# Kernel tuning notes

Measured on AMD Instinct MI355X. Metric: run time of the kernel, lower is better.

Reference implementation:

```python
import jax, jax.numpy as jnp
import numpy as np

B, T, D, C = 8, 4096, 768, 2048

def setup_inputs() -> dict:
    key = jax.random.key(0)
    k1, k2 = jax.random.split(key)
    embed = jax.random.normal(k1, (B, T, D), dtype=jnp.float32)
    cluster_centers = jax.random.normal(k2, (C, D), dtype=jnp.float32)
    return {"embed": embed, "cluster_centers": cluster_centers}

def reference(embed, cluster_centers):
    x_sq = jnp.sum(embed * embed, axis=-1, keepdims=True)          # (b, t, 1)
    c_sq = jnp.sum(cluster_centers * cluster_centers, axis=-1)     # (c,)
    cross = jnp.einsum('btd,cd->btc', embed, cluster_centers)      # (b, t, c)
    sq_dists = x_sq + c_sq[None, None, :] - 2.0 * cross
    dists = jnp.sqrt(jnp.maximum(sq_dists, 0.0))
    # dists argmax of -cdist == argmin of cdist
    clusters = jnp.argmin(dists, axis=-1)                          # (b, t) int
    return clusters
```

## Files before the change

kernel.cpp:

```cpp
#include <hip/hip_runtime.h>

typedef __fp16 f16x2 __attribute__((ext_vector_type(2)));
typedef __fp16 f16x8 __attribute__((ext_vector_type(8)));
typedef float f32x4 __attribute__((ext_vector_type(4)));

constexpr int MM = 32768;
constexpr int NN = 2048;
constexpr int KK = 768;
constexpr int BM = 128;
constexpr int BN = 128;
constexpr int NKT = KK / 32;
constexpr int NA_UNITS = (MM / 16) * NKT;
constexpr int NB_UNITS = (NN / 16) * NKT;

constexpr size_t WS_APACK = 0;
constexpr size_t WS_BPACK = WS_APACK + (size_t)MM * KK * 4;
constexpr size_t WS_CSQ   = WS_BPACK + (size_t)NN * KK * 4;
constexpr size_t WS_SLOT  = WS_CSQ + (size_t)NN * 4;
constexpr size_t WS_NEED  = WS_SLOT + (size_t)MM * 16 * 8;

__device__ __forceinline__ unsigned bc(f16x2 h) {
    return __builtin_bit_cast(unsigned, h);
}


__global__ __launch_bounds__(256)
void fragpack_kernel(const float* __restrict__ A, const float* __restrict__ Bc,
                     uint4* __restrict__ Ap, uint4* __restrict__ Bp,
                     float* __restrict__ csq) {
    const int task = blockIdx.x * 4 + (threadIdx.x >> 6);
    const int lane = threadIdx.x & 63;

    if (task >= NA_UNITS + NB_UNITS) {
        const int cl = task - (NA_UNITS + NB_UNITS);
        const float4* row = reinterpret_cast<const float4*>(Bc + (size_t)cl * KK);
        float s = 0.f;
#pragma unroll
        for (int w = 0; w < KK / (4 * 64); ++w) {
            float4 v = row[w * 64 + lane];
            s = fmaf(v.x, v.x, s); s = fmaf(v.y, v.y, s);
            s = fmaf(v.z, v.z, s); s = fmaf(v.w, v.w, s);
        }
#pragma unroll
        for (int off = 32; off > 0; off >>= 1) s += __shfl_xor(s, off, 64);
        if (lane == 0) csq[cl] = s;
        return;
    }

    const int ln15 = lane & 15;
    const int quad = lane >> 4;

    const bool isB = task >= NA_UNITS;
    const int t = isB ? task - NA_UNITS : task;
    const int tile = t / NKT, kt = t % NKT;
    const float* src = (isB ? Bc : A) + (size_t)(tile * 16 + ln15) * KK + kt * 32 + quad * 8;
    uint4* dst = (isB ? Bp : Ap) + (size_t)t * 128 + lane;

    const float4 v0 = *(const float4*)(src);
    const float4 v1 = *(const float4*)(src + 4);
    f16x2 h0 = __builtin_amdgcn_cvt_pkrtz(v0.x, v0.y);
    f16x2 h1 = __builtin_amdgcn_cvt_pkrtz(v0.z, v0.w);
    f16x2 h2 = __builtin_amdgcn_cvt_pkrtz(v1.x, v1.y);
    f16x2 h3 = __builtin_amdgcn_cvt_pkrtz(v1.z, v1.w);
    f16x2 l0 = __builtin_amdgcn_cvt_pkrtz(v0.x-(float)h0[0], v0.y-(float)h0[1]);
    f16x2 l1 = __builtin_amdgcn_cvt_pkrtz(v0.z-(float)h1[0], v0.w-(float)h1[1]);
    f16x2 l2 = __builtin_amdgcn_cvt_pkrtz(v1.x-(float)h2[0], v1.y-(float)h2[1]);
    f16x2 l3 = __builtin_amdgcn_cvt_pkrtz(v1.z-(float)h3[0], v1.w-(float)h3[1]);
    uint4 hv = {bc(h0), bc(h1), bc(h2), bc(h3)};
    uint4 lv = {bc(l0), bc(l1), bc(l2), bc(l3)};
    dst[0]  = hv;
    dst[64] = lv;
}

__global__ __launch_bounds__(64)
void csq_kernel(const float* __restrict__ cc, float* __restrict__ csq) {
    const int cl = blockIdx.x;
    const int lane = threadIdx.x;
    const float4* row = reinterpret_cast<const float4*>(cc + (size_t)cl * KK);
    float s = 0.f;
#pragma unroll
    for (int w = 0; w < KK / (4 * 64); ++w) {
        float4 v = row[w * 64 + lane];
        s = fmaf(v.x, v.x, s); s = fmaf(v.y, v.y, s);
        s = fmaf(v.z, v.z, s); s = fmaf(v.w, v.w, s);
    }
#pragma unroll
    for (int off = 32; off > 0; off >>= 1) s += __shfl_xor(s, off, 64);
    if (lane == 0) csq[cl] = s;
}

#define MF(a, b, c) __builtin_amdgcn_mfma_f32_16x16x32_f16( \
    __builtin_bit_cast(f16x8, a), __builtin_bit_cast(f16x8, b), c, 0, 0, 0)

#define COMP_J(Ah_, Al_, Bh_, Bl_, j) \
    _Pragma("unroll") \
    for (int i = 0; i < 4; ++i) { \
        acc[i][j] = MF(Ah_[i], Bh_[j], acc[i][j]); \
        acc[i][j] = MF(Ah_[i], Bl_[j], acc[i][j]); \
        acc[i][j] = MF(Al_[i], Bh_[j], acc[i][j]); \
    }

#define LOAD_B(Bh_, Bl_, kt_) { const int o_ = (kt_) * 128; \
    _Pragma("unroll") \
    for (int j = 0; j < 4; ++j) { Bh_[j] = b_ptr[j][o_]; Bl_[j] = b_ptr[j][o_ + 64]; } }

#define LOAD_A(Ah_, Al_, kt_) { const int o_ = (kt_) * 128; \
    _Pragma("unroll") \
    for (int i = 0; i < 4; ++i) { Ah_[i] = a_ptr[i][o_]; Al_[i] = a_ptr[i][o_ + 64]; } }

__global__ __launch_bounds__(256, 2)
void gemm_pack_kernel(const uint4* __restrict__ Ap, const uint4* __restrict__ Bp,
                      const float* __restrict__ csq, uint2* __restrict__ slots) {
    const int b   = blockIdx.x;
    const int xcd = b & 7;
    const int s   = b >> 3;
    const int gx  = s & 15;
    const int gy  = xcd + ((s >> 4) << 3);

    const int tid  = threadIdx.x;
    const int lane = tid & 63;
    const int ln15 = lane & 15;
    const int quad = lane >> 4;
    const int wave = tid >> 6;
    const int wm = wave >> 1, wn = wave & 1;
    const int tbase = gy * BM;
    const int cb    = gx * BN;

    const uint4* a_ptr[4];
    const uint4* b_ptr[4];
#pragma unroll
    for (int i = 0; i < 4; ++i) {
        a_ptr[i] = Ap + (size_t)(gy * 8 + wm * 4 + i) * NKT * 128 + lane;
        b_ptr[i] = Bp + (size_t)(gx * 8 + wn * 4 + i) * NKT * 128 + lane;
    }

    f32x4 acc[4][4];
#pragma unroll
    for (int i = 0; i < 4; ++i)
#pragma unroll
        for (int j = 0; j < 4; ++j) { f32x4 z = {0.f,0.f,0.f,0.f}; acc[i][j] = z; }

    uint4 Ah0[4], Al0[4], Bh0[4], Bl0[4];
    uint4 Ah1[4], Al1[4], Bh1[4], Bl1[4];

    LOAD_B(Bh0, Bl0, 0)
    LOAD_A(Ah0, Al0, 0)
#pragma unroll 1
    for (int kt = 0; kt < NKT; kt += 2) {
        LOAD_B(Bh1, Bl1, kt + 1)
        COMP_J(Ah0, Al0, Bh0, Bl0, 0)
        COMP_J(Ah0, Al0, Bh0, Bl0, 1)
        LOAD_A(Ah1, Al1, kt + 1)
        COMP_J(Ah0, Al0, Bh0, Bl0, 2)
        COMP_J(Ah0, Al0, Bh0, Bl0, 3)
        if (kt + 2 < NKT) LOAD_B(Bh0, Bl0, kt + 2)
        COMP_J(Ah1, Al1, Bh1, Bl1, 0)
        COMP_J(Ah1, Al1, Bh1, Bl1, 1)
        if (kt + 2 < NKT) LOAD_A(Ah0, Al0, kt + 2)
        COMP_J(Ah1, Al1, Bh1, Bl1, 2)
        COMP_J(Ah1, Al1, Bh1, Bl1, 3)
    }

    float csq4[4];
#pragma unroll
    for (int j = 0; j < 4; ++j) csq4[j] = csq[cb + wn * 64 + j * 16 + ln15];

    float bval[16]; int bidx[16];
#pragma unroll
    for (int i = 0; i < 4; ++i)
#pragma unroll
        for (int r = 0; r < 4; ++r) {
            const int rid = i * 4 + r;
            float bv_ = csq4[0] - 2.0f * acc[i][0][r];
            int   bi_ = cb + wn * 64 + ln15;
#pragma unroll
            for (int j = 1; j < 4; ++j) {
                const float s2 = csq4[j] - 2.0f * acc[i][j][r];
                const int   c = cb + wn * 64 + j * 16 + ln15;
                if (s2 < bv_) { bv_ = s2; bi_ = c; }
            }
            bval[rid] = bv_; bidx[rid] = bi_;
        }
#pragma unroll
    for (int off = 1; off < 16; off <<= 1) {
#pragma unroll
        for (int rid = 0; rid < 16; ++rid) {
            const float ov = __shfl_xor(bval[rid], off, 64);
            const int   oi = __shfl_xor(bidx[rid], off, 64);
            if (ov < bval[rid] || (ov == bval[rid] && oi < bidx[rid])) {
                bval[rid] = ov; bidx[rid] = oi;
            }
        }
    }

    __shared__ float vtab[256];
    __shared__ int   itab[256];
    if (ln15 == 0) {
#pragma unroll
        for (int i = 0; i < 4; ++i)
#pragma unroll
            for (int r = 0; r < 4; ++r) {
                const int row = wm * 64 + i * 16 + quad * 4 + r;
                vtab[row * 2 + wn] = bval[i * 4 + r];
                itab[row * 2 + wn] = bidx[i * 4 + r];
            }
    }
    __syncthreads();
    if (tid < 128) {
        float v0 = vtab[tid * 2]; int i0 = itab[tid * 2];
        const float v1 = vtab[tid * 2 + 1]; const int i1 = itab[tid * 2 + 1];
        if (v1 < v0 || (v1 == v0 && i1 < i0)) { v0 = v1; i0 = i1; }
        uint2 e; e.x = __float_as_uint(v0); e.y = (unsigned)i0;
        slots[(size_t)(tbase + tid) * 16 + gx] = e;
    }
}

__global__ __launch_bounds__(256)
void slot_reduce_kernel(const uint2* __restrict__ slots, int* __restrict__ out) {
    const int t = blockIdx.x * 256 + threadIdx.x;
    const uint2* s = slots + (size_t)t * 16;
    float bv = __uint_as_float(s[0].x); int bi = (int)s[0].y;
#pragma unroll
    for (int j = 1; j < 16; ++j) {
        const uint2 e = s[j];
        const float v = __uint_as_float(e.x);
        if (v < bv || (v == bv && (int)e.y < bi)) { bv = v; bi = (int)e.y; }
    }
    out[t] = bi;
}


__global__ __launch_bounds__(256)
void init_ws_kernel(unsigned long long* __restrict__ w) {
    w[blockIdx.x * 256 + threadIdx.x] = 0xFFFFFFFFFFFFFFFFull;
}

__global__ __launch_bounds__(256, 2)
void argmin_mfma_kernel(const float* __restrict__ A, const float* __restrict__ Bc,
                        const float* __restrict__ csq,
                        unsigned long long* __restrict__ ws64) {
    __shared__ unsigned lds[4 * 128 * 20];
    constexpr int AH = 0, AL = 2560, BH = 5120;

    const int tid  = threadIdx.x;
    const int lane = tid & 63;
    const int ln15 = lane & 15;
    const int quad = lane >> 4;
    const int wave = tid >> 6;
    const int wm = wave >> 1, wn = wave & 1;
    const int tbase = blockIdx.x * BM;
    const int cb    = blockIdx.y * BN;

    const int sr  = tid >> 1;
    const int skh = tid & 1;
    const float* gA = A  + (size_t)(tbase + sr) * KK + skh * 16;
    const float* gB = Bc + (size_t)(cb   + sr) * KK + skh * 16;
    const int wword = sr * 20 + skh * 8;

    f32x4 acc[4][4];
#pragma unroll
    for (int i = 0; i < 4; ++i)
#pragma unroll
        for (int j = 0; j < 4; ++j) { f32x4 z = {0.f,0.f,0.f,0.f}; acc[i][j] = z; }

    float4 av[4], bv[4];
#pragma unroll
    for (int p = 0; p < 4; ++p) {
        av[p] = *(const float4*)(gA + p * 4);
        bv[p] = *(const float4*)(gB + p * 4);
    }

    int aw[4], bw[4];
#pragma unroll
    for (int i = 0; i < 4; ++i) {
        aw[i] = AH + (wm * 64 + i * 16 + ln15) * 20 + quad * 4;
        bw[i] = BH + (wn * 64 + i * 16 + ln15) * 20 + quad * 4;
    }

    for (int k0 = 0; k0 < KK; k0 += 32) {
        __syncthreads();
#pragma unroll
        for (int h = 0; h < 2; ++h) {
            float4 v0 = av[2*h], v1 = av[2*h+1];
            f16x2 h00 = __builtin_amdgcn_cvt_pkrtz(v0.x, v0.y);
            f16x2 h01 = __builtin_amdgcn_cvt_pkrtz(v0.z, v0.w);
            f16x2 h10 = __builtin_amdgcn_cvt_pkrtz(v1.x, v1.y);
            f16x2 h11 = __builtin_amdgcn_cvt_pkrtz(v1.z, v1.w);
            f16x2 l00 = __builtin_amdgcn_cvt_pkrtz(v0.x-(float)h00[0], v0.y-(float)h00[1]);
            f16x2 l01 = __builtin_amdgcn_cvt_pkrtz(v0.z-(float)h01[0], v0.w-(float)h01[1]);
            f16x2 l10 = __builtin_amdgcn_cvt_pkrtz(v1.x-(float)h10[0], v1.y-(float)h10[1]);
            f16x2 l11 = __builtin_amdgcn_cvt_pkrtz(v1.z-(float)h11[0], v1.w-(float)h11[1]);
            uint4 hv = {bc(h00), bc(h01), bc(h10), bc(h11)};
            uint4 lv = {bc(l00), bc(l01), bc(l10), bc(l11)};
            *(uint4*)&lds[AH + wword + 4*h] = hv;
            *(uint4*)&lds[AL + wword + 4*h] = lv;

            float4 w0 = bv[2*h], w1 = bv[2*h+1];
            f16x2 g00 = __builtin_amdgcn_cvt_pkrtz(w0.x, w0.y);
            f16x2 g01 = __builtin_amdgcn_cvt_pkrtz(w0.z, w0.w);
            f16x2 g10 = __builtin_amdgcn_cvt_pkrtz(w1.x, w1.y);
            f16x2 g11 = __builtin_amdgcn_cvt_pkrtz(w1.z, w1.w);
            f16x2 m00 = __builtin_amdgcn_cvt_pkrtz(w0.x-(float)g00[0], w0.y-(float)g00[1]);
            f16x2 m01 = __builtin_amdgcn_cvt_pkrtz(w0.z-(float)g01[0], w0.w-(float)g01[1]);
            f16x2 m10 = __builtin_amdgcn_cvt_pkrtz(w1.x-(float)g10[0], w1.y-(float)g10[1]);
            f16x2 m11 = __builtin_amdgcn_cvt_pkrtz(w1.z-(float)g11[0], w1.w-(float)g11[1]);
            uint4 gv = {bc(g00), bc(g01), bc(g10), bc(g11)};
            uint4 mv = {bc(m00), bc(m01), bc(m10), bc(m11)};
            *(uint4*)&lds[BH + wword + 4*h]        = gv;
            *(uint4*)&lds[BH + 2560 + wword + 4*h] = mv;
        }
        __syncthreads();

        const int kn = k0 + 32;
        if (kn < KK) {
#pragma unroll
            for (int p = 0; p < 4; ++p) {
                av[p] = *(const float4*)(gA + kn + p * 4);
                bv[p] = *(const float4*)(gB + kn + p * 4);
            }
        }

        f16x8 a_h[4], a_l[4], b_h[4], b_l[4];
#pragma unroll
        for (int i = 0; i < 4; ++i) {
            a_h[i] = *(const f16x8*)&lds[aw[i]];
            a_l[i] = *(const f16x8*)&lds[aw[i] + 2560];
            b_h[i] = *(const f16x8*)&lds[bw[i]];
            b_l[i] = *(const f16x8*)&lds[bw[i] + 2560];
        }
#pragma unroll
        for (int i = 0; i < 4; ++i)
#pragma unroll
            for (int j = 0; j < 4; ++j) {
                acc[i][j] = __builtin_amdgcn_mfma_f32_16x16x32_f16(a_h[i], b_h[j], acc[i][j], 0, 0, 0);
                acc[i][j] = __builtin_amdgcn_mfma_f32_16x16x32_f16(a_h[i], b_l[j], acc[i][j], 0, 0, 0);
                acc[i][j] = __builtin_amdgcn_mfma_f32_16x16x32_f16(a_l[i], b_h[j], acc[i][j], 0, 0, 0);
            }
    }

    float csq4[4];
#pragma unroll
    for (int j = 0; j < 4; ++j) csq4[j] = csq[cb + wn * 64 + j * 16 + ln15];

    float bval[16]; int bidx[16];
#pragma unroll
    for (int i = 0; i < 4; ++i)
#pragma unroll
        for (int r = 0; r < 4; ++r) {
            const int rid = i * 4 + r;
            float bv_ = csq4[0] - 2.0f * acc[i][0][r];
            int   bi_ = cb + wn * 64 + ln15;
#pragma unroll
            for (int j = 1; j < 4; ++j) {
                const float s = csq4[j] - 2.0f * acc[i][j][r];
                const int   c = cb + wn * 64 + j * 16 + ln15;
                if (s < bv_) { bv_ = s; bi_ = c; }
            }
            bval[rid] = bv_; bidx[rid] = bi_;
        }
#pragma unroll
    for (int off = 1; off < 16; off <<= 1) {
#pragma unroll
        for (int rid = 0; rid < 16; ++rid) {
            const float ov = __shfl_xor(bval[rid], off, 64);
            const int   oi = __shfl_xor(bidx[rid], off, 64);
            if (ov < bval[rid] || (ov == bval[rid] && oi < bidx[rid])) {
                bval[rid] = ov; bidx[rid] = oi;
            }
        }
    }

    __syncthreads();
    float* vtab = (float*)&lds[0];
    int*   itab = (int*)&lds[256];
    if (ln15 == 0) {
#pragma unroll
        for (int i = 0; i < 4; ++i)
#pragma unroll
            for (int r = 0; r < 4; ++r) {
                const int row = wm * 64 + i * 16 + quad * 4 + r;
                vtab[row * 2 + wn] = bval[i * 4 + r];
                itab[row * 2 + wn] = bidx[i * 4 + r];
            }
    }
    __syncthreads();
    if (tid < 128) {
        float v0 = vtab[tid * 2]; int i0 = itab[tid * 2];
        const float v1 = vtab[tid * 2 + 1]; const int i1 = itab[tid * 2 + 1];
        if (v1 < v0 || (v1 == v0 && i1 < i0)) { v0 = v1; i0 = i1; }
        const unsigned b   = __float_as_uint(v0);
        const unsigned key = (b & 0x80000000u) ? ~b : (b | 0x80000000u);
        const unsigned long long pk =
            ((unsigned long long)key << 32) | (unsigned long long)(unsigned)i0;
        atomicMin(&ws64[tbase + tid], pk);
    }
}

__global__ __launch_bounds__(256)
void unpack_kernel(const unsigned long long* __restrict__ w, int* __restrict__ out) {
    const int i = blockIdx.x * 256 + threadIdx.x;
    out[i] = (int)(unsigned)(w[i] & 0xFFFFFFFFull);
}

extern "C" void kernel_launch(void* const* d_in, const int* in_sizes, int n_in,
                              void* d_out, int out_size, void* d_ws, size_t ws_size,
                              hipStream_t stream) {
    const float* embed   = (const float*)d_in[0];
    const float* centers = (const float*)d_in[1];
    int* out = (int*)d_out;

    if (ws_size >= WS_NEED) {
        uint4* Ap = (uint4*)((char*)d_ws + WS_APACK);
        uint4* Bp = (uint4*)((char*)d_ws + WS_BPACK);
        float* csq   = (float*)((char*)d_ws + WS_CSQ);
        uint2* slots = (uint2*)((char*)d_ws + WS_SLOT);
        fragpack_kernel<<<(NA_UNITS + NB_UNITS + NN) / 4, 256, 0, stream>>>(
            embed, centers, Ap, Bp, csq);
        gemm_pack_kernel<<<(MM / BM) * (NN / BN), 256, 0, stream>>>(
            Ap, Bp, csq, slots);
        slot_reduce_kernel<<<MM / 256, 256, 0, stream>>>(slots, out);
    } else {
        unsigned long long* ws64 = (unsigned long long*)d_ws;
        float* csq = (float*)((char*)d_ws + (size_t)MM * 8);
        init_ws_kernel<<<MM / 256, 256, 0, stream>>>(ws64);
        csq_kernel<<<NN, 64, 0, stream>>>(centers, csq);
        argmin_mfma_kernel<<<dim3(MM / BM, NN / BN), 256, 0, stream>>>(
            embed, centers, csq, ws64);
        unpack_kernel<<<MM / 256, 256, 0, stream>>>(ws64, out);
    }
}
```

Before: 441.2 us.

## Use 256x256 LDS-staged tiles with async global-to-LDS double buffering in GEMM

The packed-fragment GEMM moves from 128x128 tiles, where each wave loads its fragments directly from global memory, to 256x256 tiles with 512 threads. Fragments are staged cooperatively into double-buffered LDS via global_load_lds, and each wave then reads them from LDS to feed the MFMAs. The goal is to cut global/L2 traffic through more reuse per tile and to overlap the next k-tile load with compute, with s_setprio to favour the MFMA issue. The cost is two barriers per k-step, higher register pressure from 8x4 accumulators, and fewer blocks, which may hurt occupancy and load balance. Column slots per row drop from 16 to 8, so the reduce kernel is adjusted to match.

Measured after the change: 429.0 us. 2.8% less time.

```diff
diff --git a/kernel.cpp b/kernel.cpp
--- a/kernel.cpp
+++ b/kernel.cpp
@@ -7,8 +7,6 @@
 constexpr int MM = 32768;
 constexpr int NN = 2048;
 constexpr int KK = 768;
-constexpr int BM = 128;
-constexpr int BN = 128;
 constexpr int NKT = KK / 32;
 constexpr int NA_UNITS = (MM / 16) * NKT;
 constexpr int NB_UNITS = (NN / 16) * NKT;
@@ -17,7 +15,7 @@
 constexpr size_t WS_BPACK = WS_APACK + (size_t)MM * KK * 4;
 constexpr size_t WS_CSQ   = WS_BPACK + (size_t)NN * KK * 4;
 constexpr size_t WS_SLOT  = WS_CSQ + (size_t)NN * 4;
-constexpr size_t WS_NEED  = WS_SLOT + (size_t)MM * 16 * 8;
+constexpr size_t WS_NEED  = WS_SLOT + (size_t)MM * 8 * 8;
 
 __device__ __forceinline__ unsigned bc(f16x2 h) {
     return __builtin_bit_cast(unsigned, h);
@@ -89,33 +87,196 @@
     if (lane == 0) csq[cl] = s;
 }
 
-#define MF(a, b, c) __builtin_amdgcn_mfma_f32_16x16x32_f16( \
-    __builtin_bit_cast(f16x8, a), __builtin_bit_cast(f16x8, b), c, 0, 0, 0)
-
-#define COMP_J(Ah_, Al_, Bh_, Bl_, j) \
-    _Pragma("unroll") \
-    for (int i = 0; i < 4; ++i) { \
-        acc[i][j] = MF(Ah_[i], Bh_[j], acc[i][j]); \
-        acc[i][j] = MF(Ah_[i], Bl_[j], acc[i][j]); \
-        acc[i][j] = MF(Al_[i], Bh_[j], acc[i][j]); \
-    }
-
-#define LOAD_B(Bh_, Bl_, kt_) { const int o_ = (kt_) * 128; \
-    _Pragma("unroll") \
-    for (int j = 0; j < 4; ++j) { Bh_[j] = b_ptr[j][o_]; Bl_[j] = b_ptr[j][o_ + 64]; } }
-
-#define LOAD_A(Ah_, Al_, kt_) { const int o_ = (kt_) * 128; \
-    _Pragma("unroll") \
-    for (int i = 0; i < 4; ++i) { Ah_[i] = a_ptr[i][o_]; Al_[i] = a_ptr[i][o_ + 64]; } }
-
-__global__ __launch_bounds__(256, 2)
+#define MF2(a, b, c) __builtin_amdgcn_mfma_f32_16x16x32_f16(a, b, c, 0, 0, 0)
+
+__global__ __launch_bounds__(512, 2)
 void gemm_pack_kernel(const uint4* __restrict__ Ap, const uint4* __restrict__ Bp,
                       const float* __restrict__ csq, uint2* __restrict__ slots) {
+    __shared__ uint4 ldsq[8192];
+
     const int b   = blockIdx.x;
     const int xcd = b & 7;
     const int s   = b >> 3;
-    const int gx  = s & 15;
-    const int gy  = xcd + ((s >> 4) << 3);
+    const int gy  = xcd * 16 + (s >> 3);
+    const int gx  = s & 7;
+
+    const int tid  = threadIdx.x;
+    const int lane = tid & 63;
+    const int ln15 = lane & 15;
+    const int quad = lane >> 4;
+    const int wave = tid >> 6;
+    const int wm   = wave >> 2;
+    const int wn   = wave & 3;
+    const int tbase = gy * 256;
+    const int cb    = gx * 256;
+
+    const uint4* sp[8];
+#pragma unroll
+    for (int q = 0; q < 8; ++q) {
+        const int u = wave * 8 + q;
+        const bool isA = u < 32;
+        const int v = isA ? u : u - 32;
+        const int tile = (isA ? gy * 16 : gx * 16) + (v >> 1);
+        const int part = v & 1;
+        sp[q] = (isA ? Ap : Bp) + (size_t)tile * NKT * 128 + part * 64 + lane;
+    }
+    const int myunit = wave * 8 * 64;
+
+    auto STAGE = [&](int kt, int bufq) {
+#pragma unroll
+        for (int q = 0; q < 8; ++q) {
+            __builtin_amdgcn_global_load_lds(
+                (const __attribute__((address_space(1))) unsigned int*)(sp[q] + kt * 128),
+                (__attribute__((address_space(3))) unsigned int*)&ldsq[bufq + myunit + q * 64],
+                16, 0, 0);
+        }
+    };
+
+    f32x4 acc[8][4];
+#pragma unroll
+    for (int i = 0; i < 8; ++i)
+#pragma unroll
+        for (int j = 0; j < 4; ++j) { f32x4 z = {0.f,0.f,0.f,0.f}; acc[i][j] = z; }
+
+    STAGE(0, 0);
+
+    auto BODY = [&](int kt, int bufq, int nxtq, bool stage_next) {
+        if (stage_next) {
+            STAGE(kt + 1, nxtq);
+            asm volatile("s_waitcnt vmcnt(8)" ::: "memory");
+        } else {
+            asm volatile("s_waitcnt vmcnt(0)" ::: "memory");
+        }
+        __builtin_amdgcn_sched_barrier(0);
+        __builtin_amdgcn_s_barrier();
+        __builtin_amdgcn_sched_barrier(0);
+
+        f16x8 Bh[4], Bl[4];
+#pragma unroll
+        for (int j = 0; j < 4; ++j) {
+            const int nu = (wn * 4 + j) * 2;
+            Bh[j] = *(const f16x8*)&ldsq[bufq + 2048 + nu * 64 + lane];
+            Bl[j] = *(const f16x8*)&ldsq[bufq + 2048 + (nu + 1) * 64 + lane];
+        }
+#pragma unroll
+        for (int p = 0; p < 4; ++p) {
+            f16x8 Ah[2], Al[2];
+#pragma unroll
+            for (int t2 = 0; t2 < 2; ++t2) {
+                const int au = (wm * 8 + p * 2 + t2) * 2;
+                Ah[t2] = *(const f16x8*)&ldsq[bufq + au * 64 + lane];
+                Al[t2] = *(const f16x8*)&ldsq[bufq + (au + 1) * 64 + lane];
+            }
+            __builtin_amdgcn_s_setprio(1);
+#pragma unroll
+            for (int t2 = 0; t2 < 2; ++t2) {
+                const int i = p * 2 + t2;
+#pragma unroll
+                for (int j = 0; j < 4; ++j) {
+                    acc[i][j] = MF2(Ah[t2], Bh[j], acc[i][j]);
+                    acc[i][j] = MF2(Ah[t2], Bl[j], acc[i][j]);
+                    acc[i][j] = MF2(Al[t2], Bh[j], acc[i][j]);
+                }
+            }
+            __builtin_amdgcn_s_setprio(0);
+        }
+        __builtin_amdgcn_sched_barrier(0);
+        __builtin_amdgcn_s_barrier();
+        __builtin_amdgcn_sched_barrier(0);
+    };
+
+#pragma unroll 1
+    for (int kt = 0; kt < NKT - 2; kt += 2) {
+        BODY(kt,     0,    4096, true);
+        BODY(kt + 1, 4096, 0,    true);
+    }
+    BODY(NKT - 2, 0,    4096, true);
+    BODY(NKT - 1, 4096, 0,    false);
+
+    float csq4[4];
+#pragma unroll
+    for (int j = 0; j < 4; ++j) csq4[j] = csq[cb + wn * 64 + j * 16 + ln15];
+
+    float bval[32]; int bidx[32];
+#pragma unroll
+    for (int i = 0; i < 8; ++i)
+#pragma unroll
+        for (int r = 0; r < 4; ++r) {
+            const int rid = i * 4 + r;
+            float bv_ = csq4[0] - 2.0f * acc[i][0][r];
+            int   bi_ = cb + wn * 64 + ln15;
+#pragma unroll
+            for (int j = 1; j < 4; ++j) {
+                const float s2 = csq4[j] - 2.0f * acc[i][j][r];
+                const int   c = cb + wn * 64 + j * 16 + ln15;
+                if (s2 < bv_) { bv_ = s2; bi_ = c; }
+            }
+            bval[rid] = bv_; bidx[rid] = bi_;
+        }
+#pragma unroll
+    for (int off = 1; off < 16; off <<= 1) {
+#pragma unroll
+        for (int rid = 0; rid < 32; ++rid) {
+            const float ov = __shfl_xor(bval[rid], off, 64);
+            const int   oi = __shfl_xor(bidx[rid], off, 64);
+            if (ov < bval[rid] || (ov == bval[rid] && oi < bidx[rid])) {
+                bval[rid] = ov; bidx[rid] = oi;
+            }
+        }
+    }
+
+    __syncthreads();
+    float* vtab = (float*)&ldsq[0];
+    int*   itab = (int*)&ldsq[256];
+    if (ln15 == 0) {
+#pragma unroll
+        for (int i = 0; i < 8; ++i)
+#pragma unroll
+            for (int r = 0; r < 4; ++r) {
+                const int row = wm * 128 + i * 16 + quad * 4 + r;
+                vtab[row * 4 + wn] = bval[i * 4 + r];
+                itab[row * 4 + wn] = bidx[i * 4 + r];
+            }
+    }
+    __syncthreads();
+    if (tid < 256) {
+        float v0 = vtab[tid * 4]; int i0 = itab[tid * 4];
+#pragma unroll
+        for (int e = 1; e < 4; ++e) {
+            const float v1 = vtab[tid * 4 + e]; const int i1 = itab[tid * 4 + e];
+            if (v1 < v0 || (v1 == v0 && i1 < i0)) { v0 = v1; i0 = i1; }
+        }
+        uint2 e; e.x = __float_as_uint(v0); e.y = (unsigned)i0;
+        slots[(size_t)(tbase + tid) * 8 + gx] = e;
+    }
+}
+
+__global__ __launch_bounds__(256)
+void slot_reduce_kernel(const uint2* __restrict__ slots, int* __restrict__ out) {
+    const int t = blockIdx.x * 256 + threadIdx.x;
+    const uint2* s = slots + (size_t)t * 8;
+    float bv = __uint_as_float(s[0].x); int bi = (int)s[0].y;
+#pragma unroll
+    for (int j = 1; j < 8; ++j) {
+        const uint2 e = s[j];
+        const float v = __uint_as_float(e.x);
+        if (v < bv || (v == bv && (int)e.y < bi)) { bv = v; bi = (int)e.y; }
+    }
+    out[t] = bi;
+}
+
+
+__global__ __launch_bounds__(256)
+void init_ws_kernel(unsigned long long* __restrict__ w) {
+    w[blockIdx.x * 256 + threadIdx.x] = 0xFFFFFFFFFFFFFFFFull;
+}
+
+__global__ __launch_bounds__(256, 2)
+void argmin_mfma_kernel(const float* __restrict__ A, const float* __restrict__ Bc,
+                        const float* __restrict__ csq,
+                        unsigned long long* __restrict__ ws64) {
+    __shared__ unsigned lds[4 * 128 * 20];
+    constexpr int AH = 0, AL = 2560, BH = 5120;
 
     const int tid  = threadIdx.x;
     const int lane = tid & 63;
@@ -123,133 +284,8 @@
     const int quad = lane >> 4;
     const int wave = tid >> 6;
     const int wm = wave >> 1, wn = wave & 1;
-    const int tbase = gy * BM;
-    const int cb    = gx * BN;
-
-    const uint4* a_ptr[4];
-    const uint4* b_ptr[4];
-#pragma unroll
-    for (int i = 0; i < 4; ++i) {
-        a_ptr[i] = Ap + (size_t)(gy * 8 + wm * 4 + i) * NKT * 128 + lane;
-        b_ptr[i] = Bp + (size_t)(gx * 8 + wn * 4 + i) * NKT * 128 + lane;
-    }
-
-    f32x4 acc[4][4];
-#pragma unroll
-    for (int i = 0; i < 4; ++i)
-#pragma unroll
-        for (int j = 0; j < 4; ++j) { f32x4 z = {0.f,0.f,0.f,0.f}; acc[i][j] = z; }
-
-    uint4 Ah0[4], Al0[4], Bh0[4], Bl0[4];
-    uint4 Ah1[4], Al1[4], Bh1[4], Bl1[4];
-
-    LOAD_B(Bh0, Bl0, 0)
-    LOAD_A(Ah0, Al0, 0)
-#pragma unroll 1
-    for (int kt = 0; kt < NKT; kt += 2) {
-        LOAD_B(Bh1, Bl1, kt + 1)
-        COMP_J(Ah0, Al0, Bh0, Bl0, 0)
-        COMP_J(Ah0, Al0, Bh0, Bl0, 1)
-        LOAD_A(Ah1, Al1, kt + 1)
-        COMP_J(Ah0, Al0, Bh0, Bl0, 2)
-        COMP_J(Ah0, Al0, Bh0, Bl0, 3)
-        if (kt + 2 < NKT) LOAD_B(Bh0, Bl0, kt + 2)
-        COMP_J(Ah1, Al1, Bh1, Bl1, 0)
-        COMP_J(Ah1, Al1, Bh1, Bl1, 1)
-        if (kt + 2 < NKT) LOAD_A(Ah0, Al0, kt + 2)
-        COMP_J(Ah1, Al1, Bh1, Bl1, 2)
-        COMP_J(Ah1, Al1, Bh1, Bl1, 3)
-    }
-
-    float csq4[4];
-#pragma unroll
-    for (int j = 0; j < 4; ++j) csq4[j] = csq[cb + wn * 64 + j * 16 + ln15];
-
-    float bval[16]; int bidx[16];
-#pragma unroll
-    for (int i = 0; i < 4; ++i)
-#pragma unroll
-        for (int r = 0; r < 4; ++r) {
-            const int rid = i * 4 + r;
-            float bv_ = csq4[0] - 2.0f * acc[i][0][r];
-            int   bi_ = cb + wn * 64 + ln15;
-#pragma unroll
-            for (int j = 1; j < 4; ++j) {
-                const float s2 = csq4[j] - 2.0f * acc[i][j][r];
-                const int   c = cb + wn * 64 + j * 16 + ln15;
-                if (s2 < bv_) { bv_ = s2; bi_ = c; }
-            }
-            bval[rid] = bv_; bidx[rid] = bi_;
-        }
-#pragma unroll
-    for (int off = 1; off < 16; off <<= 1) {
-#pragma unroll
-        for (int rid = 0; rid < 16; ++rid) {
-            const float ov = __shfl_xor(bval[rid], off, 64);
-            const int   oi = __shfl_xor(bidx[rid], off, 64);
-            if (ov < bval[rid] || (ov == bval[rid] && oi < bidx[rid])) {
-                bval[rid] = ov; bidx[rid] = oi;
-            }
-        }
-    }
-
-    __shared__ float vtab[256];
-    __shared__ int   itab[256];
-    if (ln15 == 0) {
-#pragma unroll
-        for (int i = 0; i < 4; ++i)
-#pragma unroll
-            for (int r = 0; r < 4; ++r) {
-                const int row = wm * 64 + i * 16 + quad * 4 + r;
-                vtab[row * 2 + wn] = bval[i * 4 + r];
-                itab[row * 2 + wn] = bidx[i * 4 + r];
-            }
-    }
-    __syncthreads();
-    if (tid < 128) {
-        float v0 = vtab[tid * 2]; int i0 = itab[tid * 2];
-        const float v1 = vtab[tid * 2 + 1]; const int i1 = itab[tid * 2 + 1];
-        if (v1 < v0 || (v1 == v0 && i1 < i0)) { v0 = v1; i0 = i1; }
-        uint2 e; e.x = __float_as_uint(v0); e.y = (unsigned)i0;
-        slots[(size_t)(tbase + tid) * 16 + gx] = e;
-    }
-}
-
-__global__ __launch_bounds__(256)
-void slot_reduce_kernel(const uint2* __restrict__ slots, int* __restrict__ out) {
-    const int t = blockIdx.x * 256 + threadIdx.x;
-    const uint2* s = slots + (size_t)t * 16;
-    float bv = __uint_as_float(s[0].x); int bi = (int)s[0].y;
-#pragma unroll
-    for (int j = 1; j < 16; ++j) {
-        const uint2 e = s[j];
-        const float v = __uint_as_float(e.x);
-        if (v < bv || (v == bv && (int)e.y < bi)) { bv = v; bi = (int)e.y; }
-    }
-    out[t] = bi;
-}
-
-
-__global__ __launch_bounds__(256)
-void init_ws_kernel(unsigned long long* __restrict__ w) {
-    w[blockIdx.x * 256 + threadIdx.x] = 0xFFFFFFFFFFFFFFFFull;
-}
-
-__global__ __launch_bounds__(256, 2)
-void argmin_mfma_kernel(const float* __restrict__ A, const float* __restrict__ Bc,
-                        const float* __restrict__ csq,
-                        unsigned long long* __restrict__ ws64) {
-    __shared__ unsigned lds[4 * 128 * 20];
-    constexpr int AH = 0, AL = 2560, BH = 5120;
-
-    const int tid  = threadIdx.x;
-    const int lane = tid & 63;
-    const int ln15 = lane & 15;
-    const int quad = lane >> 4;
-    const int wave = tid >> 6;
-    const int wm = wave >> 1, wn = wave & 1;
-    const int tbase = blockIdx.x * BM;
-    const int cb    = blockIdx.y * BN;
+    const int tbase = blockIdx.x * 128;
+    const int cb    = blockIdx.y * 128;
 
     const int sr  = tid >> 1;
     const int skh = tid & 1;
@@ -416,7 +452,7 @@
         uint2* slots = (uint2*)((char*)d_ws + WS_SLOT);
         fragpack_kernel<<<(NA_UNITS + NB_UNITS + NN) / 4, 256, 0, stream>>>(
             embed, centers, Ap, Bp, csq);
-        gemm_pack_kernel<<<(MM / BM) * (NN / BN), 256, 0, stream>>>(
+        gemm_pack_kernel<<<(MM / 256) * (NN / 256), 512, 0, stream>>>(
             Ap, Bp, csq, slots);
         slot_reduce_kernel<<<MM / 256, 256, 0, stream>>>(slots, out);
     } else {
@@ -424,7 +460,7 @@
         float* csq = (float*)((char*)d_ws + (size_t)MM * 8);
         init_ws_kernel<<<MM / 256, 256, 0, stream>>>(ws64);
         csq_kernel<<<NN, 64, 0, stream>>>(centers, csq);
-        argmin_mfma_kernel<<<dim3(MM / BM, NN / BN), 256, 0, stream>>>(
+        argmin_mfma_kernel<<<dim3(MM / 128, NN / 128), 256, 0, stream>>>(
             embed, centers, csq, ws64);
         unpack_kernel<<<MM / 256, 256, 0, stream>>>(ws64, out);
     }
```

## Stage packed GEMM fragments through LDS with async global_load_lds double buffering

Applied to the files above, without the earlier changes.

In the GEMM kernel, each wave used to load its own A/B fragments straight from global memory into registers. Now the block cooperatively stages the packed A and B fragments into a double-buffered LDS area with global_load_lds and reads them back from LDS for the MFMAs. The goal is to share loads across waves instead of each wave fetching overlapping B and A tiles, and to overlap the next k-tile's load with the current compute using explicit vmcnt waits, sched barriers and setprio. The cost is two block barriers per k-step and a 64KB LDS footprint, which may limit occupancy to two blocks per CU.

Result: no change. 443.7 us (+0.6%).

```diff
diff --git a/kernel.cpp b/kernel.cpp
--- a/kernel.cpp
+++ b/kernel.cpp
@@ -7,8 +7,6 @@
 constexpr int MM = 32768;
 constexpr int NN = 2048;
 constexpr int KK = 768;
-constexpr int BM = 128;
-constexpr int BN = 128;
 constexpr int NKT = KK / 32;
 constexpr int NA_UNITS = (MM / 16) * NKT;
 constexpr int NB_UNITS = (NN / 16) * NKT;
@@ -89,28 +87,14 @@
     if (lane == 0) csq[cl] = s;
 }
 
-#define MF(a, b, c) __builtin_amdgcn_mfma_f32_16x16x32_f16( \
-    __builtin_bit_cast(f16x8, a), __builtin_bit_cast(f16x8, b), c, 0, 0, 0)
-
-#define COMP_J(Ah_, Al_, Bh_, Bl_, j) \
-    _Pragma("unroll") \
-    for (int i = 0; i < 4; ++i) { \
-        acc[i][j] = MF(Ah_[i], Bh_[j], acc[i][j]); \
-        acc[i][j] = MF(Ah_[i], Bl_[j], acc[i][j]); \
-        acc[i][j] = MF(Al_[i], Bh_[j], acc[i][j]); \
-    }
-
-#define LOAD_B(Bh_, Bl_, kt_) { const int o_ = (kt_) * 128; \
-    _Pragma("unroll") \
-    for (int j = 0; j < 4; ++j) { Bh_[j] = b_ptr[j][o_]; Bl_[j] = b_ptr[j][o_ + 64]; } }
-
-#define LOAD_A(Ah_, Al_, kt_) { const int o_ = (kt_) * 128; \
-    _Pragma("unroll") \
-    for (int i = 0; i < 4; ++i) { Ah_[i] = a_ptr[i][o_]; Al_[i] = a_ptr[i][o_ + 64]; } }
+#define MF2(a, b, c) __builtin_amdgcn_mfma_f32_16x16x32_f16(a, b, c, 0, 0, 0)
+#define DSB() __builtin_amdgcn_sched_barrier(0)
 
 __global__ __launch_bounds__(256, 2)
 void gemm_pack_kernel(const uint4* __restrict__ Ap, const uint4* __restrict__ Bp,
                       const float* __restrict__ csq, uint2* __restrict__ slots) {
+    __shared__ uint4 ldsq[4096];
+
     const int b   = blockIdx.x;
     const int xcd = b & 7;
     const int s   = b >> 3;
@@ -122,17 +106,29 @@
     const int ln15 = lane & 15;
     const int quad = lane >> 4;
     const int wave = tid >> 6;
-    const int wm = wave >> 1, wn = wave & 1;
-    const int tbase = gy * BM;
-    const int cb    = gx * BN;
-
-    const uint4* a_ptr[4];
-    const uint4* b_ptr[4];
-#pragma unroll
-    for (int i = 0; i < 4; ++i) {
-        a_ptr[i] = Ap + (size_t)(gy * 8 + wm * 4 + i) * NKT * 128 + lane;
-        b_ptr[i] = Bp + (size_t)(gx * 8 + wn * 4 + i) * NKT * 128 + lane;
-    }
+    const int wm   = wave >> 1;
+    const int wn   = wave & 1;
+    const int tbase = gy * 128;
+    const int cb    = gx * 128;
+
+    const uint4* sp[8];
+#pragma unroll
+    for (int q = 0; q < 8; ++q) {
+        const int u = wave * 8 + q;
+        const bool isA = u < 16;
+        const int v = isA ? u : u - 16;
+        const int tile = (isA ? gy * 8 : gx * 8) + (v >> 1);
+        const int part = v & 1;
+        sp[q] = (isA ? Ap : Bp) + (size_t)tile * NKT * 128 + part * 64 + lane;
+    }
+
+#define STAGE2(kt_, bufq_, q_) {                                              \
+    _Pragma("unroll")                                                         \
+    for (int qq = (q_); qq < (q_) + 2; ++qq)                                  \
+        __builtin_amdgcn_global_load_lds(                                     \
+            (const __attribute__((address_space(1))) unsigned int*)(sp[qq] + (kt_) * 128), \
+            (__attribute__((address_space(3))) unsigned int*)&ldsq[(bufq_) + (wave * 8 + qq) * 64], \
+            16, 0, 0); }
 
     f32x4 acc[4][4];
 #pragma unroll
@@ -140,25 +136,68 @@
 #pragma unroll
         for (int j = 0; j < 4; ++j) { f32x4 z = {0.f,0.f,0.f,0.f}; acc[i][j] = z; }
 
-    uint4 Ah0[4], Al0[4], Bh0[4], Bl0[4];
-    uint4 Ah1[4], Al1[4], Bh1[4], Bl1[4];
-
-    LOAD_B(Bh0, Bl0, 0)
-    LOAD_A(Ah0, Al0, 0)
+    f16x8 Bh[4], Bl[4];
+    f16x8 Ah[2], Al[2];
+
+#define RD_B(bufq_) {                                                         \
+    _Pragma("unroll")                                                         \
+    for (int j = 0; j < 4; ++j) {                                             \
+        const int nu = 16 + (wn * 4 + j) * 2;                                 \
+        Bh[j] = *(const f16x8*)&ldsq[(bufq_) + nu * 64 + lane];               \
+        Bl[j] = *(const f16x8*)&ldsq[(bufq_) + (nu + 1) * 64 + lane];         \
+    } }
+
+#define RD_A(bufq_, i_, s_) {                                                 \
+    const int au = (wm * 4 + (i_)) * 2;                                       \
+    Ah[s_] = *(const f16x8*)&ldsq[(bufq_) + au * 64 + lane];                  \
+    Al[s_] = *(const f16x8*)&ldsq[(bufq_) + (au + 1) * 64 + lane]; }
+
+#define MFMA_I(i_, s_) {                                                      \
+    __builtin_amdgcn_s_setprio(1);                                            \
+    _Pragma("unroll")                                                         \
+    for (int j = 0; j < 4; ++j) {                                             \
+        acc[i_][j] = MF2(Ah[s_], Bh[j], acc[i_][j]);                          \
+        acc[i_][j] = MF2(Ah[s_], Bl[j], acc[i_][j]);                          \
+        acc[i_][j] = MF2(Al[s_], Bh[j], acc[i_][j]);                          \
+    }                                                                         \
+    __builtin_amdgcn_s_setprio(0); }
+
+    STAGE2(0, 0, 0) STAGE2(0, 0, 2) STAGE2(0, 0, 4) STAGE2(0, 0, 6)
+
 #pragma unroll 1
-    for (int kt = 0; kt < NKT; kt += 2) {
-        LOAD_B(Bh1, Bl1, kt + 1)
-        COMP_J(Ah0, Al0, Bh0, Bl0, 0)
-        COMP_J(Ah0, Al0, Bh0, Bl0, 1)
-        LOAD_A(Ah1, Al1, kt + 1)
-        COMP_J(Ah0, Al0, Bh0, Bl0, 2)
-        COMP_J(Ah0, Al0, Bh0, Bl0, 3)
-        if (kt + 2 < NKT) LOAD_B(Bh0, Bl0, kt + 2)
-        COMP_J(Ah1, Al1, Bh1, Bl1, 0)
-        COMP_J(Ah1, Al1, Bh1, Bl1, 1)
-        if (kt + 2 < NKT) LOAD_A(Ah0, Al0, kt + 2)
-        COMP_J(Ah1, Al1, Bh1, Bl1, 2)
-        COMP_J(Ah1, Al1, Bh1, Bl1, 3)
+    for (int kt = 0; kt < NKT; ++kt) {
+        const int bufq = (kt & 1) ? 2048 : 0;
+        const int nxt  = bufq ^ 2048;
+        const bool sn  = (kt + 1 < NKT);
+
+        if (sn) {
+            STAGE2(kt + 1, nxt, 0)
+            asm volatile("s_waitcnt vmcnt(2)" ::: "memory");
+        } else {
+            asm volatile("s_waitcnt vmcnt(0)" ::: "memory");
+        }
+        DSB(); __builtin_amdgcn_s_barrier(); DSB();
+
+        RD_B(bufq)
+        RD_A(bufq, 0, 0)
+        DSB();
+        RD_A(bufq, 1, 1)
+        if (sn) STAGE2(kt + 1, nxt, 2)
+        DSB();
+        MFMA_I(0, 0)
+        DSB();
+        RD_A(bufq, 2, 0)
+        if (sn) STAGE2(kt + 1, nxt, 4)
+        DSB();
+        MFMA_I(1, 1)
+        DSB();
+        RD_A(bufq, 3, 1)
+        if (sn) STAGE2(kt + 1, nxt, 6)
+        DSB();
+        MFMA_I(2, 0)
+        DSB();
+        MFMA_I(3, 1)
+        DSB(); __builtin_amdgcn_s_barrier(); DSB();
     }
 
     float csq4[4];
@@ -193,8 +232,9 @@
         }
     }
 
-    __shared__ float vtab[256];
-    __shared__ int   itab[256];
+    __syncthreads();
+    float* vtab = (float*)&ldsq[0];
+    int*   itab = (int*)&ldsq[64];
     if (ln15 == 0) {
 #pragma unroll
         for (int i = 0; i < 4; ++i)
@@ -248,8 +288,8 @@
     const int quad = lane >> 4;
     const int wave = tid >> 6;
     const int wm = wave >> 1, wn = wave & 1;
-    const int tbase = blockIdx.x * BM;
-    const int cb    = blockIdx.y * BN;
+    const int tbase = blockIdx.x * 128;
+    const int cb    = blockIdx.y * 128;
 
     const int sr  = tid >> 1;
     const int skh = tid & 1;
@@ -416,7 +456,7 @@
         uint2* slots = (uint2*)((char*)d_ws + WS_SLOT);
         fragpack_kernel<<<(NA_UNITS + NB_UNITS + NN) / 4, 256, 0, stream>>>(
             embed, centers, Ap, Bp, csq);
-        gemm_pack_kernel<<<(MM / BM) * (NN / BN), 256, 0, stream>>>(
+        gemm_pack_kernel<<<(MM / 128) * (NN / 128), 256, 0, stream>>>(
             Ap, Bp, csq, slots);
         slot_reduce_kernel<<<MM / 256, 256, 0, stream>>>(slots, out);
     } else {
@@ -424,7 +464,7 @@
         float* csq = (float*)((char*)d_ws + (size_t)MM * 8);
         init_ws_kernel<<<MM / 256, 256, 0, stream>>>(ws64);
         csq_kernel<<<NN, 64, 0, stream>>>(centers, csq);
-        argmin_mfma_kernel<<<dim3(MM / BM, NN / BN), 256, 0, stream>>>(
+        argmin_mfma_kernel<<<dim3(MM / 128, NN / 128), 256, 0, stream>>>(
             embed, centers, csq, ws64);
         unpack_kernel<<<MM / 256, 256, 0, stream>>>(ws64, out);
     }
```
